# Kernel tuning notes

Measured on AMD Instinct MI355X. Metric: run time of the kernel, lower is better.

The kernel has to match this reference:

```python
import jax, jax.numpy as jnp
import numpy as np

N_NODES = 100000
N_EDGES = 3200000
D_NODE = 128
D_EDGE = 16


def setup_inputs() -> dict:
    key = jax.random.key(0)
    k1, k2, k3, k4, k5, k6, k7 = jax.random.split(key, 7)
    nodes = jax.random.normal(k1, (N_NODES, D_NODE), dtype=jnp.float32)
    edges = jax.random.normal(k2, (N_EDGES, D_EDGE), dtype=jnp.float32)
    senders = jax.random.randint(k3, (N_EDGES,), 0, N_NODES, dtype=jnp.int32)
    receivers = jax.random.randint(k4, (N_EDGES,), 0, N_NODES, dtype=jnp.int32)
    w_node = jax.random.normal(k5, (), dtype=jnp.float32)
    w_edge = jax.random.normal(k6, (), dtype=jnp.float32)
    b_node = jax.random.normal(k7, (), dtype=jnp.float32)
    return {
        "nodes": nodes,
        "edges": edges,
        "senders": senders,
        "receivers": receivers,
        "w_node": w_node,
        "w_edge": w_edge,
        "b_node": b_node,
    }


def reference(nodes, edges, senders, receivers, w_node, w_edge, b_node):
    # gather sender node scalar feature (column 0): [E]
    sender_vals = nodes[senders, 0]
    edge_vals = edges[:, 0]  # [E]
    # per-edge message: scalar mult-add
    messages = w_edge * edge_vals + w_node * sender_vals  # [E]
    # scatter-add into receivers: [N]
    agg = jax.ops.segment_sum(messages, receivers, num_segments=nodes.shape[0])
    return w_node * nodes[:, 0] + agg + b_node
```

## Files before the change

kernel.cpp:

```cpp
#include <hip/hip_runtime.h>

#define N_NODES 100000
#define N_EDGES 3200000
#define D_NODE 128
#define D_EDGE 16

#define RANGE_BITS 14
#define RANGE_SIZE (1 << RANGE_BITS)
#define RANGE_MASK (RANGE_SIZE - 1)
#define N_RANGES 7

#define WS_X_OFF    0
#define WS_MSG_OFF  102400
#define WS_PART_OFF (102400 + N_EDGES)

__global__ void tmp_k0_extract(const float* __restrict__ nodes,
                               float* __restrict__ x) {
    int i = blockIdx.x * blockDim.x + threadIdx.x;
    if (i < N_NODES) x[i] = nodes[(size_t)i * D_NODE];
}

__global__ void tmp_k1_messages(const float* __restrict__ x,
                                const float* __restrict__ edges,
                                const int*   __restrict__ senders,
                                const float* __restrict__ w_node,
                                const float* __restrict__ w_edge,
                                float* __restrict__ msg) {
    const float wn = w_node[0];
    const float we = w_edge[0];
    int base = (blockIdx.x * blockDim.x + threadIdx.x) * 4;
    if (base >= N_EDGES) return;
    int4 s = *(const int4*)(senders + base);
    float4 m;
    m.x = we * edges[(size_t)(base + 0) * D_EDGE] + wn * x[s.x];
    m.y = we * edges[(size_t)(base + 1) * D_EDGE] + wn * x[s.y];
    m.z = we * edges[(size_t)(base + 2) * D_EDGE] + wn * x[s.z];
    m.w = we * edges[(size_t)(base + 3) * D_EDGE] + wn * x[s.w];
    *(float4*)(msg + base) = m;
}

__global__ void tmp_k2_accum(const float* __restrict__ msg,
                             const int*   __restrict__ receivers,
                             float* __restrict__ partials, int nb) {
    extern __shared__ float acc[];
    const int range = blockIdx.y;
    const int slice = blockIdx.x;

    for (int i = threadIdx.x; i < RANGE_SIZE; i += blockDim.x) acc[i] = 0.f;
    __syncthreads();

    int chunk = (N_EDGES + nb - 1) / nb;
    chunk = (chunk + 3) & ~3;
    int start = slice * chunk;
    int end = start + chunk; if (end > N_EDGES) end = N_EDGES;

    for (int e = start + (int)threadIdx.x * 4; e < end; e += (int)blockDim.x * 4) {
        int4 r = *(const int4*)(receivers + e);
        float4 m = *(const float4*)(msg + e);
        if ((r.x >> RANGE_BITS) == range) atomicAdd(&acc[r.x & RANGE_MASK], m.x);
        if ((r.y >> RANGE_BITS) == range) atomicAdd(&acc[r.y & RANGE_MASK], m.y);
        if ((r.z >> RANGE_BITS) == range) atomicAdd(&acc[r.z & RANGE_MASK], m.z);
        if ((r.w >> RANGE_BITS) == range) atomicAdd(&acc[r.w & RANGE_MASK], m.w);
    }
    __syncthreads();

    float* dst = partials + ((size_t)(range * nb + slice) << RANGE_BITS);
    for (int i = threadIdx.x; i < RANGE_SIZE; i += blockDim.x) dst[i] = acc[i];
}

__global__ void tmp_k3_reduce(const float* __restrict__ x,
                              const float* __restrict__ partials,
                              const float* __restrict__ w_node,
                              const float* __restrict__ b_node,
                              float* __restrict__ out, int nb) {
    int i = blockIdx.x * blockDim.x + threadIdx.x;
    if (i >= N_NODES) return;
    int range = i >> RANGE_BITS;
    int local = i & RANGE_MASK;
    float s = w_node[0] * x[i] + b_node[0];
    const float* p = partials + ((size_t)(range * nb) << RANGE_BITS) + local;
    for (int b = 0; b < nb; ++b) s += p[(size_t)b << RANGE_BITS];
    out[i] = s;
}

__global__ void tmp_init_out(const float* __restrict__ nodes,
                             const float* __restrict__ w_node,
                             const float* __restrict__ b_node,
                             float* __restrict__ out) {
    int i = blockIdx.x * blockDim.x + threadIdx.x;
    if (i < N_NODES) out[i] = w_node[0] * nodes[(size_t)i * D_NODE] + b_node[0];
}

__global__ void tmp_edge_scatter_direct(const float* __restrict__ nodes,
                                        const float* __restrict__ edges,
                                        const int*   __restrict__ senders,
                                        const int*   __restrict__ receivers,
                                        const float* __restrict__ w_node,
                                        const float* __restrict__ w_edge,
                                        float* __restrict__ out) {
    const float wn = w_node[0];
    const float we = w_edge[0];
    int base = (blockIdx.x * blockDim.x + threadIdx.x) * 4;
    if (base + 3 < N_EDGES) {
        int4 s = *(const int4*)(senders + base);
        int4 r = *(const int4*)(receivers + base);
        atomicAdd(&out[r.x], we * edges[(size_t)(base + 0) * D_EDGE] + wn * nodes[(size_t)s.x * D_NODE]);
        atomicAdd(&out[r.y], we * edges[(size_t)(base + 1) * D_EDGE] + wn * nodes[(size_t)s.y * D_NODE]);
        atomicAdd(&out[r.z], we * edges[(size_t)(base + 2) * D_EDGE] + wn * nodes[(size_t)s.z * D_NODE]);
        atomicAdd(&out[r.w], we * edges[(size_t)(base + 3) * D_EDGE] + wn * nodes[(size_t)s.w * D_NODE]);
    } else {
        for (int e = base; e < N_EDGES; ++e) {
            atomicAdd(&out[receivers[e]],
                      we * edges[(size_t)e * D_EDGE] + wn * nodes[(size_t)senders[e] * D_NODE]);
        }
    }
}

extern "C" void kernel_launch(void* const* d_in, const int* in_sizes, int n_in,
                              void* d_out, int out_size, void* d_ws, size_t ws_size,
                              hipStream_t stream) {
    const float* nodes     = (const float*)d_in[0];
    const float* edges     = (const float*)d_in[1];
    const int*   senders   = (const int*)d_in[2];
    const int*   receivers = (const int*)d_in[3];
    const float* w_node    = (const float*)d_in[4];
    const float* w_edge    = (const float*)d_in[5];
    const float* b_node    = (const float*)d_in[6];
    float* out = (float*)d_out;
    float* ws  = (float*)d_ws;

    int nb = 0;
    for (int cand : {64, 48, 32, 16, 8}) {
        size_t need = ((size_t)WS_PART_OFF +
                       (size_t)N_RANGES * cand * RANGE_SIZE) * sizeof(float);
        if (ws_size >= need) { nb = cand; break; }
    }

    if (nb > 0) {
        float* x        = ws + WS_X_OFF;
        float* msg      = ws + WS_MSG_OFF;
        float* partials = ws + WS_PART_OFF;
        int threads = 256;

        tmp_k0_extract<<<(N_NODES + threads - 1) / threads, threads, 0, stream>>>(
            nodes, x);

        int n_thr = N_EDGES / 4;
        tmp_k1_messages<<<(n_thr + threads - 1) / threads, threads, 0, stream>>>(
            x, edges, senders, w_node, w_edge, msg);

        dim3 grid2(nb, N_RANGES);
        tmp_k2_accum<<<grid2, threads, RANGE_SIZE * sizeof(float), stream>>>(
            msg, receivers, partials, nb);

        tmp_k3_reduce<<<(N_NODES + threads - 1) / threads, threads, 0, stream>>>(
            x, partials, w_node, b_node, out, nb);
    } else {
        int threads = 256;
        tmp_init_out<<<(N_NODES + threads - 1) / threads, threads, 0, stream>>>(
            nodes, w_node, b_node, out);
        int n_thr = N_EDGES / 4;
        tmp_edge_scatter_direct<<<(n_thr + threads - 1) / threads, threads, 0, stream>>>(
            nodes, edges, senders, receivers, w_node, w_edge, out);
    }
}
```

Measured before the change: 388.5 us.

## Bucket edges by receiver range before shared-memory accumulation

The message kernel now computes each edge message and also writes a (local index, message) pair into a per-range bucket. It claims bucket slots with shared-memory counters plus one global atomic per range per block. The accumulation kernel then reads only its own range's bucket, instead of every block scanning all receivers and messages seven times. This cuts the repeated full-edge reads. The cost is a much larger workspace for seven edge-sized pair buffers; if the workspace is too small, the slow direct-atomic fallback runs instead. Slice count and block sizes are also fixed at new constants.

```diff
diff --git a/kernel.cpp b/kernel.cpp
--- a/kernel.cpp
+++ b/kernel.cpp
@@ -6,80 +6,121 @@
 #define D_EDGE 16
 
 #define RANGE_BITS 14
-#define RANGE_SIZE (1 << RANGE_BITS)
-#define RANGE_MASK (RANGE_SIZE - 1)
+#define RANGE_SIZE 16384
+#define RANGE_MASK 16383
 #define N_RANGES 7
-
-#define WS_X_OFF    0
-#define WS_MSG_OFF  102400
-#define WS_PART_OFF (102400 + N_EDGES)
+#define NB 73
+
+#define K1_THREADS 512
+#define K1_EPT 8
+#define K1_TILE (K1_THREADS * K1_EPT)
+
+#define WS_X      0
+#define WS_GCNT   102400
+#define WS_PAIRS  102432
+#define WS_PART   (102432 + 2 * N_RANGES * N_EDGES)
+#define WS_TOTAL  (WS_PART + N_RANGES * NB * RANGE_SIZE)
 
 __global__ void tmp_k0_extract(const float* __restrict__ nodes,
-                               float* __restrict__ x) {
+                               float* __restrict__ x,
+                               int* __restrict__ gcnt) {
     int i = blockIdx.x * blockDim.x + threadIdx.x;
     if (i < N_NODES) x[i] = nodes[(size_t)i * D_NODE];
-}
-
-__global__ void tmp_k1_messages(const float* __restrict__ x,
-                                const float* __restrict__ edges,
-                                const int*   __restrict__ senders,
-                                const float* __restrict__ w_node,
-                                const float* __restrict__ w_edge,
-                                float* __restrict__ msg) {
+    if (i < N_RANGES) gcnt[i] = 0;
+}
+
+__global__ __launch_bounds__(K1_THREADS) void tmp_k1_partition(
+        const float* __restrict__ x,
+        const float* __restrict__ edges,
+        const int*   __restrict__ senders,
+        const int*   __restrict__ receivers,
+        const float* __restrict__ w_node,
+        const float* __restrict__ w_edge,
+        int* __restrict__ gcnt,
+        int2* __restrict__ pairs) {
+    __shared__ int lcnt[N_RANGES];
+    __shared__ int lbase[N_RANGES];
+    if (threadIdx.x < N_RANGES) lcnt[threadIdx.x] = 0;
+    __syncthreads();
+
     const float wn = w_node[0];
     const float we = w_edge[0];
-    int base = (blockIdx.x * blockDim.x + threadIdx.x) * 4;
-    if (base >= N_EDGES) return;
-    int4 s = *(const int4*)(senders + base);
-    float4 m;
-    m.x = we * edges[(size_t)(base + 0) * D_EDGE] + wn * x[s.x];
-    m.y = we * edges[(size_t)(base + 1) * D_EDGE] + wn * x[s.y];
-    m.z = we * edges[(size_t)(base + 2) * D_EDGE] + wn * x[s.z];
-    m.w = we * edges[(size_t)(base + 3) * D_EDGE] + wn * x[s.w];
-    *(float4*)(msg + base) = m;
-}
-
-__global__ void tmp_k2_accum(const float* __restrict__ msg,
-                             const int*   __restrict__ receivers,
-                             float* __restrict__ partials, int nb) {
-    extern __shared__ float acc[];
+    const int e0 = blockIdx.x * K1_TILE + (int)threadIdx.x * K1_EPT;
+    const bool active = e0 < N_EDGES;
+
+    int   b[K1_EPT], off[K1_EPT], loc[K1_EPT];
+    float msg[K1_EPT];
+    if (active) {
+        int4 s0 = *(const int4*)(senders + e0);
+        int4 s1 = *(const int4*)(senders + e0 + 4);
+        int4 r0 = *(const int4*)(receivers + e0);
+        int4 r1 = *(const int4*)(receivers + e0 + 4);
+        int ss[K1_EPT] = {s0.x, s0.y, s0.z, s0.w, s1.x, s1.y, s1.z, s1.w};
+        int rr[K1_EPT] = {r0.x, r0.y, r0.z, r0.w, r1.x, r1.y, r1.z, r1.w};
+#pragma unroll
+        for (int j = 0; j < K1_EPT; ++j) {
+            float ev = __builtin_nontemporal_load(edges + (size_t)(e0 + j) * D_EDGE);
+            msg[j] = we * ev + wn * x[ss[j]];
+            b[j]   = rr[j] >> RANGE_BITS;
+            loc[j] = rr[j] & RANGE_MASK;
+            off[j] = atomicAdd(&lcnt[b[j]], 1);
+        }
+    }
+    __syncthreads();
+    if (threadIdx.x < N_RANGES)
+        lbase[threadIdx.x] = atomicAdd(&gcnt[threadIdx.x], lcnt[threadIdx.x]);
+    __syncthreads();
+    if (active) {
+#pragma unroll
+        for (int j = 0; j < K1_EPT; ++j) {
+            int2 p;
+            p.x = loc[j];
+            p.y = __float_as_int(msg[j]);
+            pairs[(size_t)b[j] * N_EDGES + (size_t)(lbase[b[j]] + off[j])] = p;
+        }
+    }
+}
+
+__global__ __launch_bounds__(1024) void tmp_k2_accum(
+        const int2* __restrict__ pairs,
+        const int*  __restrict__ gcnt,
+        float* __restrict__ partials) {
+    __shared__ float acc[RANGE_SIZE];
     const int range = blockIdx.y;
     const int slice = blockIdx.x;
 
-    for (int i = threadIdx.x; i < RANGE_SIZE; i += blockDim.x) acc[i] = 0.f;
-    __syncthreads();
-
-    int chunk = (N_EDGES + nb - 1) / nb;
-    chunk = (chunk + 3) & ~3;
+    for (int i = threadIdx.x; i < RANGE_SIZE; i += 1024) acc[i] = 0.f;
+    __syncthreads();
+
+    const int n = gcnt[range];
+    int chunk = (n + NB - 1) / NB;
     int start = slice * chunk;
-    int end = start + chunk; if (end > N_EDGES) end = N_EDGES;
-
-    for (int e = start + (int)threadIdx.x * 4; e < end; e += (int)blockDim.x * 4) {
-        int4 r = *(const int4*)(receivers + e);
-        float4 m = *(const float4*)(msg + e);
-        if ((r.x >> RANGE_BITS) == range) atomicAdd(&acc[r.x & RANGE_MASK], m.x);
-        if ((r.y >> RANGE_BITS) == range) atomicAdd(&acc[r.y & RANGE_MASK], m.y);
-        if ((r.z >> RANGE_BITS) == range) atomicAdd(&acc[r.z & RANGE_MASK], m.z);
-        if ((r.w >> RANGE_BITS) == range) atomicAdd(&acc[r.w & RANGE_MASK], m.w);
-    }
-    __syncthreads();
-
-    float* dst = partials + ((size_t)(range * nb + slice) << RANGE_BITS);
-    for (int i = threadIdx.x; i < RANGE_SIZE; i += blockDim.x) dst[i] = acc[i];
+    int end = start + chunk; if (end > n) end = n;
+    const int2* src = pairs + (size_t)range * N_EDGES;
+
+    for (int i = start + (int)threadIdx.x; i < end; i += 1024) {
+        int2 p = src[i];
+        atomicAdd(&acc[p.x], __int_as_float(p.y));
+    }
+    __syncthreads();
+
+    float* dst = partials + ((size_t)(range * NB + slice) << RANGE_BITS);
+    for (int i = threadIdx.x; i < RANGE_SIZE; i += 1024) dst[i] = acc[i];
 }
 
 __global__ void tmp_k3_reduce(const float* __restrict__ x,
                               const float* __restrict__ partials,
                               const float* __restrict__ w_node,
                               const float* __restrict__ b_node,
-                              float* __restrict__ out, int nb) {
+                              float* __restrict__ out) {
     int i = blockIdx.x * blockDim.x + threadIdx.x;
     if (i >= N_NODES) return;
     int range = i >> RANGE_BITS;
     int local = i & RANGE_MASK;
     float s = w_node[0] * x[i] + b_node[0];
-    const float* p = partials + ((size_t)(range * nb) << RANGE_BITS) + local;
-    for (int b = 0; b < nb; ++b) s += p[(size_t)b << RANGE_BITS];
+    const float* p = partials + (((size_t)range * NB) << RANGE_BITS) + local;
+#pragma unroll 4
+    for (int bq = 0; bq < NB; ++bq) s += p[(size_t)bq << RANGE_BITS];
     out[i] = s;
 }
 
@@ -129,32 +170,25 @@
     float* out = (float*)d_out;
     float* ws  = (float*)d_ws;
 
-    int nb = 0;
-    for (int cand : {64, 48, 32, 16, 8}) {
-        size_t need = ((size_t)WS_PART_OFF +
-                       (size_t)N_RANGES * cand * RANGE_SIZE) * sizeof(float);
-        if (ws_size >= need) { nb = cand; break; }
-    }
-
-    if (nb > 0) {
-        float* x        = ws + WS_X_OFF;
-        float* msg      = ws + WS_MSG_OFF;
-        float* partials = ws + WS_PART_OFF;
+    if (ws_size >= (size_t)WS_TOTAL * sizeof(float)) {
+        float* x        = ws + WS_X;
+        int*   gcnt     = (int*)(ws + WS_GCNT);
+        int2*  pairs    = (int2*)(ws + WS_PAIRS);
+        float* partials = ws + WS_PART;
+
         int threads = 256;
-
         tmp_k0_extract<<<(N_NODES + threads - 1) / threads, threads, 0, stream>>>(
-            nodes, x);
-
-        int n_thr = N_EDGES / 4;
-        tmp_k1_messages<<<(n_thr + threads - 1) / threads, threads, 0, stream>>>(
-            x, edges, senders, w_node, w_edge, msg);
-
-        dim3 grid2(nb, N_RANGES);
-        tmp_k2_accum<<<grid2, threads, RANGE_SIZE * sizeof(float), stream>>>(
-            msg, receivers, partials, nb);
+            nodes, x, gcnt);
+
+        int k1_blocks = (N_EDGES + K1_TILE - 1) / K1_TILE;
+        tmp_k1_partition<<<k1_blocks, K1_THREADS, 0, stream>>>(
+            x, edges, senders, receivers, w_node, w_edge, gcnt, pairs);
+
+        dim3 grid2(NB, N_RANGES);
+        tmp_k2_accum<<<grid2, 1024, 0, stream>>>(pairs, gcnt, partials);
 
         tmp_k3_reduce<<<(N_NODES + threads - 1) / threads, threads, 0, stream>>>(
-            x, partials, w_node, b_node, out, nb);
+            x, partials, w_node, b_node, out);
     } else {
         int threads = 256;
         tmp_init_out<<<(N_NODES + threads - 1) / threads, threads, 0, stream>>>(
```

New measurement: 402.3 us. 3.5% more time.

## Widen LDS scatter ranges, use 1024-thread accum blocks, and batch message edges

Applied to the files above, without the earlier changes.

The shared-memory accumulation kernel now tries 32K-entry (128 KB) LDS ranges, which cuts the number of passes over receivers and messages from seven to four. It runs with 1024-thread blocks and a fixed 64-slice split, and falls back to 16K ranges if the larger LDS size cannot be set. The message kernel handles 8 edges per thread with 512-thread blocks and reads the edge column with nontemporal loads. The reduce loop is partially unrolled. Larger LDS per block lowers occupancy, and the change drops the workspace-size cascade in favour of a single fixed NB=64.

```diff
diff --git a/kernel.cpp b/kernel.cpp
--- a/kernel.cpp
+++ b/kernel.cpp
@@ -5,14 +5,16 @@
 #define D_NODE 128
 #define D_EDGE 16
 
-#define RANGE_BITS 14
-#define RANGE_SIZE (1 << RANGE_BITS)
-#define RANGE_MASK (RANGE_SIZE - 1)
-#define N_RANGES 7
+#define NB 64
 
-#define WS_X_OFF    0
-#define WS_MSG_OFF  102400
-#define WS_PART_OFF (102400 + N_EDGES)
+#define K1_THREADS 512
+#define K1_EPT 8
+#define K1_TILE (K1_THREADS * K1_EPT)
+
+#define WS_X      0
+#define WS_MSG    102400
+#define WS_PART   (102400 + N_EDGES)
+#define WS_TOTAL  (WS_PART + 4 * NB * 32768)
 
 __global__ void tmp_k0_extract(const float* __restrict__ nodes,
                                float* __restrict__ x) {
@@ -20,66 +22,74 @@
     if (i < N_NODES) x[i] = nodes[(size_t)i * D_NODE];
 }
 
-__global__ void tmp_k1_messages(const float* __restrict__ x,
-                                const float* __restrict__ edges,
-                                const int*   __restrict__ senders,
-                                const float* __restrict__ w_node,
-                                const float* __restrict__ w_edge,
-                                float* __restrict__ msg) {
+__global__ __launch_bounds__(K1_THREADS) void tmp_k1_messages(
+        const float* __restrict__ x,
+        const float* __restrict__ edges,
+        const int*   __restrict__ senders,
+        const float* __restrict__ w_node,
+        const float* __restrict__ w_edge,
+        float* __restrict__ msg) {
     const float wn = w_node[0];
     const float we = w_edge[0];
-    int base = (blockIdx.x * blockDim.x + threadIdx.x) * 4;
-    if (base >= N_EDGES) return;
-    int4 s = *(const int4*)(senders + base);
-    float4 m;
-    m.x = we * edges[(size_t)(base + 0) * D_EDGE] + wn * x[s.x];
-    m.y = we * edges[(size_t)(base + 1) * D_EDGE] + wn * x[s.y];
-    m.z = we * edges[(size_t)(base + 2) * D_EDGE] + wn * x[s.z];
-    m.w = we * edges[(size_t)(base + 3) * D_EDGE] + wn * x[s.w];
-    *(float4*)(msg + base) = m;
+    const int e0 = blockIdx.x * K1_TILE + (int)threadIdx.x * K1_EPT;
+    if (e0 >= N_EDGES) return;
+    int4 s0 = *(const int4*)(senders + e0);
+    int4 s1 = *(const int4*)(senders + e0 + 4);
+    int ss[K1_EPT] = {s0.x, s0.y, s0.z, s0.w, s1.x, s1.y, s1.z, s1.w};
+    float m[K1_EPT];
+#pragma unroll
+    for (int j = 0; j < K1_EPT; ++j) {
+        float ev = __builtin_nontemporal_load(edges + (size_t)(e0 + j) * D_EDGE);
+        m[j] = we * ev + wn * x[ss[j]];
+    }
+    *(float4*)(msg + e0)     = make_float4(m[0], m[1], m[2], m[3]);
+    *(float4*)(msg + e0 + 4) = make_float4(m[4], m[5], m[6], m[7]);
 }
 
-__global__ void tmp_k2_accum(const float* __restrict__ msg,
-                             const int*   __restrict__ receivers,
-                             float* __restrict__ partials, int nb) {
+__global__ __launch_bounds__(1024) void tmp_k2_accum(
+        const float* __restrict__ msg,
+        const int*   __restrict__ receivers,
+        float* __restrict__ partials,
+        int range_bits) {
     extern __shared__ float acc[];
+    const int range_size = 1 << range_bits;
+    const int range_mask = range_size - 1;
     const int range = blockIdx.y;
     const int slice = blockIdx.x;
 
-    for (int i = threadIdx.x; i < RANGE_SIZE; i += blockDim.x) acc[i] = 0.f;
+    for (int i = threadIdx.x; i < range_size; i += 1024) acc[i] = 0.f;
     __syncthreads();
 
-    int chunk = (N_EDGES + nb - 1) / nb;
-    chunk = (chunk + 3) & ~3;
-    int start = slice * chunk;
-    int end = start + chunk; if (end > N_EDGES) end = N_EDGES;
-
-    for (int e = start + (int)threadIdx.x * 4; e < end; e += (int)blockDim.x * 4) {
-        int4 r = *(const int4*)(receivers + e);
+    const int start = slice * (N_EDGES / NB);
+    const int end   = start + (N_EDGES / NB);
+    for (int e = start + (int)threadIdx.x * 4; e < end; e += 1024 * 4) {
+        int4   r = *(const int4*)(receivers + e);
         float4 m = *(const float4*)(msg + e);
-        if ((r.x >> RANGE_BITS) == range) atomicAdd(&acc[r.x & RANGE_MASK], m.x);
-        if ((r.y >> RANGE_BITS) == range) atomicAdd(&acc[r.y & RANGE_MASK], m.y);
-        if ((r.z >> RANGE_BITS) == range) atomicAdd(&acc[r.z & RANGE_MASK], m.z);
-        if ((r.w >> RANGE_BITS) == range) atomicAdd(&acc[r.w & RANGE_MASK], m.w);
+        if ((r.x >> range_bits) == range) atomicAdd(&acc[r.x & range_mask], m.x);
+        if ((r.y >> range_bits) == range) atomicAdd(&acc[r.y & range_mask], m.y);
+        if ((r.z >> range_bits) == range) atomicAdd(&acc[r.z & range_mask], m.z);
+        if ((r.w >> range_bits) == range) atomicAdd(&acc[r.w & range_mask], m.w);
     }
     __syncthreads();
 
-    float* dst = partials + ((size_t)(range * nb + slice) << RANGE_BITS);
-    for (int i = threadIdx.x; i < RANGE_SIZE; i += blockDim.x) dst[i] = acc[i];
+    float* dst = partials + ((size_t)(range * NB + slice) << range_bits);
+    for (int i = threadIdx.x; i < range_size; i += 1024) dst[i] = acc[i];
 }
 
 __global__ void tmp_k3_reduce(const float* __restrict__ x,
                               const float* __restrict__ partials,
                               const float* __restrict__ w_node,
                               const float* __restrict__ b_node,
-                              float* __restrict__ out, int nb) {
+                              float* __restrict__ out,
+                              int range_bits) {
     int i = blockIdx.x * blockDim.x + threadIdx.x;
     if (i >= N_NODES) return;
-    int range = i >> RANGE_BITS;
-    int local = i & RANGE_MASK;
+    int range = i >> range_bits;
+    int local = i & ((1 << range_bits) - 1);
     float s = w_node[0] * x[i] + b_node[0];
-    const float* p = partials + ((size_t)(range * nb) << RANGE_BITS) + local;
-    for (int b = 0; b < nb; ++b) s += p[(size_t)b << RANGE_BITS];
+    const float* p = partials + (((size_t)range * NB) << range_bits) + local;
+#pragma unroll 4
+    for (int b = 0; b < NB; ++b) s += p[(size_t)b << range_bits];
     out[i] = s;
 }
 
@@ -129,32 +139,35 @@
     float* out = (float*)d_out;
     float* ws  = (float*)d_ws;
 
-    int nb = 0;
-    for (int cand : {64, 48, 32, 16, 8}) {
-        size_t need = ((size_t)WS_PART_OFF +
-                       (size_t)N_RANGES * cand * RANGE_SIZE) * sizeof(float);
-        if (ws_size >= need) { nb = cand; break; }
-    }
+    if (ws_size >= (size_t)WS_TOTAL * sizeof(float)) {
+        float* x        = ws + WS_X;
+        float* msg      = ws + WS_MSG;
+        float* partials = ws + WS_PART;
 
-    if (nb > 0) {
-        float* x        = ws + WS_X_OFF;
-        float* msg      = ws + WS_MSG_OFF;
-        float* partials = ws + WS_PART_OFF;
+        int range_bits = 15, n_ranges = 4;
+        size_t lds_bytes = (size_t)(1 << range_bits) * sizeof(float);
+        hipError_t attr_ok = hipFuncSetAttribute(
+            reinterpret_cast<const void*>(tmp_k2_accum),
+            hipFuncAttributeMaxDynamicSharedMemorySize, (int)lds_bytes);
+        if (attr_ok != hipSuccess) {
+            range_bits = 14; n_ranges = 7;
+            lds_bytes = (size_t)(1 << range_bits) * sizeof(float);
+        }
+
         int threads = 256;
-
         tmp_k0_extract<<<(N_NODES + threads - 1) / threads, threads, 0, stream>>>(
             nodes, x);
 
-        int n_thr = N_EDGES / 4;
-        tmp_k1_messages<<<(n_thr + threads - 1) / threads, threads, 0, stream>>>(
+        int k1_blocks = (N_EDGES + K1_TILE - 1) / K1_TILE;
+        tmp_k1_messages<<<k1_blocks, K1_THREADS, 0, stream>>>(
             x, edges, senders, w_node, w_edge, msg);
 
-        dim3 grid2(nb, N_RANGES);
-        tmp_k2_accum<<<grid2, threads, RANGE_SIZE * sizeof(float), stream>>>(
-            msg, receivers, partials, nb);
+        dim3 grid2(NB, n_ranges);
+        tmp_k2_accum<<<grid2, 1024, lds_bytes, stream>>>(
+            msg, receivers, partials, range_bits);
 
         tmp_k3_reduce<<<(N_NODES + threads - 1) / threads, threads, 0, stream>>>(
-            x, partials, w_node, b_node, out, nb);
+            x, partials, w_node, b_node, out, range_bits);
     } else {
         int threads = 256;
         tmp_init_out<<<(N_NODES + threads - 1) / threads, threads, 0, stream>>>(
```

New measurement: 366.2 us. 5.7% less time.
